# Kernel optimization log

Hardware: AMD Instinct MI355X
Metric: run time of the kernel (lower is better)

## Reference

```python
import jax, jax.numpy as jnp
import numpy as np
from jax import lax
import math

B, C, L, H, K, NCONV = 64, 128, 400, 8, 7, 4  # batch, d_model, length, n_head, kernel, n_conv
DK = C // H
EPS = 1e-5


def setup_inputs() -> dict:
    key = jax.random.key(0)
    ks = jax.random.split(key, 16)
    inp = {
        'x': jax.random.normal(ks[0], (B, C, L), dtype=jnp.float32),
        'mask': jnp.ones((B, L), dtype=jnp.float32),
        'dw_w': jax.random.normal(ks[1], (NCONV, C, 1, K), dtype=jnp.float32) * 0.1,
        'dw_b': jnp.zeros((NCONV, C), dtype=jnp.float32),
        'pw_w': jax.random.normal(ks[2], (NCONV, C, C, 1), dtype=jnp.float32) * 0.05,
        'pw_b': jnp.zeros((NCONV, C), dtype=jnp.float32),
        'wq': jax.random.normal(ks[3], (C, C), dtype=jnp.float32) * 0.05,
        'bq': jnp.zeros((C,), dtype=jnp.float32),
        'wk': jax.random.normal(ks[4], (C, C), dtype=jnp.float32) * 0.05,
        'bk': jnp.zeros((C,), dtype=jnp.float32),
        'wv': jax.random.normal(ks[5], (C, C), dtype=jnp.float32) * 0.05,
        'bv': jnp.zeros((C,), dtype=jnp.float32),
        'wo': jax.random.normal(ks[6], (C, C), dtype=jnp.float32) * 0.05,
        'bo': jnp.zeros((C,), dtype=jnp.float32),
        'fc_w': jax.random.normal(ks[7], (C, C), dtype=jnp.float32) * 0.05,
        'fc_b': jnp.zeros((C,), dtype=jnp.float32),
        'ln_g': jnp.ones((C, L), dtype=jnpp.float32) if False else jnp.ones((C, L), dtype=jnp.float32),
        'ln_b': jnp.zeros((C, L), dtype=jnp.float32),
    }
    return inp


def _pos_encoding():
    i = jnp.arange(C, dtype=jnp.float32)
    even = (jnp.arange(C) % 2) == 0
    freqs = jnp.where(even, 10000.0 ** (-i / C), -(10000.0 ** ((1.0 - i) / C)))
    phases = jnp.where(even, 0.0, math.pi / 2.0)
    pos = jnp.arange(L, dtype=jnp.float32)
    return jnp.sin(pos[None, :] * freqs[:, None] + phases[:, None])  # (C, L)


def _layer_norm(o, g, b):
    # torch LayerNorm([d_model, length]): normalize each sample over (C, L) jointly
    mu = jnp.mean(o, axis=(1, 2), keepdims=True)
    var = jnp.mean((o - mu) ** 2, axis=(1, 2), keepdims=True)
    return (o - mu) * lax.rsqrt(var + EPS) * g[None] + b[None]


def _dwsep_conv(o, dw, db, pw, pb):
    # depthwise: groups=C, kernel (C,1,K), 'same' padding
    y = lax.conv_general_dilated(o, dw, window_strides=(1,), padding=[(K // 2, K // 2)],
                                 dimension_numbers=('NCH', 'OIH', 'NCH'), feature_group_count=C)
    y = y + db[None, :, None]
    # pointwise 1x1 conv
    y = jnp.einsum('oc,bcl->bol', pw[:, :, 0], y) + pb[None, :, None]
    return y


def _attention(o, mask, wq, bq, wk, bk, wv, bv, wo, bo):
    xt = jnp.transpose(o, (0, 2, 1))  # (B, L, C)
    q = (xt @ wq.T + bq).reshape(B, L, H, DK)
    k = (xt @ wk.T + bk).reshape(B, L, H, DK)
    v = (xt @ wv.T + bv).reshape(B, L, H, DK)
    atten = jnp.einsum('blhd,bmhd->bhlm', q, k) / math.sqrt(C)  # note: sqrt(d_model), faithful
    m = mask[:, None, None, :]  # (B,1,1,L)
    atten = atten * m + (1.0 - m) * -1e30
    atten = jax.nn.softmax(atten, axis=-1)
    out = jnp.einsum('bhlm,bmhd->blhd', atten, v).reshape(B, L, C)
    out = out @ wo.T + bo
    return jnp.transpose(out, (0, 2, 1))  # (B, C, L)


def reference(x, mask, dw_w, dw_b, pw_w, pw_b, wq, bq, wk, bk, wv, bv, wo, bo, fc_w, fc_b, ln_g, ln_b):
    out = x + _pos_encoding()[None]
    res = out
    out = _layer_norm(out, ln_g, ln_b)
    for i in range(NCONV):
        out = _dwsep_conv(out, dw_w[i], dw_b[i], pw_w[i], pw_b[i])
        out = jax.nn.relu(out)
        out = res + out
        res = out
        out = _layer_norm(out, ln_g, ln_b)
    out = _attention(out, mask, wq, bq, wk, bk, wv, bv, wo, bo)
    out = res + out
    res = out
    out = _layer_norm(out, ln_g, ln_b)
    out = jnp.einsum('bcl,ec->bel', out, fc_w) + fc_b[None, :, None]
    out = jax.nn.relu(out)
    out = res + out
    return out
```

## Files before the change

### kernel.cpp

```cpp
#include <hip/hip_runtime.h>
#include <math.h>

constexpr int BN = 64;
constexpr int CC = 128;
constexpr int LL = 400;
constexpr int DK = 16;
constexpr int KK = 7;
constexpr int CL = CC * LL;
constexpr int NBCL = BN * CL;
constexpr float EPSV = 1e-5f;
constexpr float INV_N = 1.0f / (float)CL;
constexpr float BIGL = 1.4427e30f;

typedef __attribute__((ext_vector_type(8))) short bf16x8;
typedef __attribute__((ext_vector_type(4))) float f32x4;

__device__ __forceinline__ short f2bf(float f) {
  unsigned u = __builtin_bit_cast(unsigned, f);
  u = (u + 0x7fffu + ((u >> 16) & 1u)) >> 16;
  return (short)u;
}
__device__ __forceinline__ unsigned pkbf(float hi, float lo) {
  return __builtin_amdgcn_perm(__builtin_bit_cast(unsigned, hi),
                               __builtin_bit_cast(unsigned, lo), 0x07060302u);
}

__global__ __launch_bounds__(256) void prep_kernel(
    const float* __restrict__ pw_w, const float* __restrict__ wq,
    const float* __restrict__ wk, const float* __restrict__ wv,
    const float* __restrict__ wo, const float* __restrict__ fcw,
    const float* __restrict__ pw_b, const float* __restrict__ dw_b,
    const float* __restrict__ mask,
    unsigned short* __restrict__ wf, float* __restrict__ pose,
    float* __restrict__ stats, float* __restrict__ beff,
    float* __restrict__ maddb)
{
  int blk = blockIdx.x;
  if (blk < 576) {
    int idx = blk * 256 + threadIdx.x;
    int mat = idx >> 14;
    int e = idx & 16383;
    const float* src;
    if (mat < 4)       src = pw_w + mat * 16384;
    else if (mat == 4) src = wq;
    else if (mat == 5) src = wk;
    else if (mat == 6) src = wv;
    else if (mat == 7) src = wo;
    else               src = fcw;
    int o = e >> 7, c = e & 127;
    int t = (o >> 4) * 4 + (c >> 5);
    int quad = (c >> 3) & 3, col = o & 15, j = c & 7;
    wf[mat * 16384 + t * 512 + (quad * 16 + col) * 8 + j] = (unsigned short)f2bf(src[e]);
  } else if (blk < 776) {
    int idx = (blk - 576) * 256 + threadIdx.x;
    int c = idx / LL, l = idx - c * LL;
    float fc = (float)c;
    float freq, ph;
    if ((c & 1) == 0) { freq = powf(10000.f, -fc / (float)CC);        ph = 0.f; }
    else              { freq = -powf(10000.f, (1.f - fc) / (float)CC); ph = 1.5707963267948966f; }
    pose[idx] = sinf((float)l * freq + ph);
  } else if (blk == 776) {
    for (int i = threadIdx.x; i < 1024; i += 256) stats[i] = 0.f;
  } else if (blk == 777) {
    for (int t = threadIdx.x; t < 512; t += 256) {
      int i = t >> 7, o = t & 127;
      float a = pw_b[t];
      const float* wrow = pw_w + (size_t)i * 16384 + o * 128;
      const float* db = dw_b + i * 128;
      for (int c2 = 0; c2 < 128; c2++) a += wrow[c2] * db[c2];
      beff[t] = a;
    }
  } else {
    int idx = (blk - 778) * 256 + threadIdx.x;
    int b = idx / 416, m = idx - b * 416;
    maddb[idx] = (m < LL) ? (mask[b * LL + m] - 1.f) * BIGL : -BIGL;
  }
}

__global__ __launch_bounds__(256) void addpos_stats_kernel(
    const float* __restrict__ x, const float* __restrict__ pose,
    float* __restrict__ res, float* __restrict__ stats)
{
  int idx4 = blockIdx.x * 256 + threadIdx.x;
  int b = idx4 / (CL / 4);
  int cl4 = (idx4 - b * (CL / 4)) * 4;
  const float4 xv = *reinterpret_cast<const float4*>(&x[(size_t)idx4 * 4]);
  const float4 pv = *reinterpret_cast<const float4*>(&pose[cl4]);
  float4 v = make_float4(xv.x + pv.x, xv.y + pv.y, xv.z + pv.z, xv.w + pv.w);
  *reinterpret_cast<float4*>(&res[(size_t)idx4 * 4]) = v;
  float s1 = v.x + v.y + v.z + v.w;
  float s2 = v.x * v.x + v.y * v.y + v.z * v.z + v.w * v.w;
  #pragma unroll
  for (int off = 32; off > 0; off >>= 1) {
    s1 += __shfl_down(s1, off);
    s2 += __shfl_down(s2, off);
  }
  __shared__ float r1[4], r2[4];
  int wv = threadIdx.x >> 6, lane = threadIdx.x & 63;
  if (lane == 0) { r1[wv] = s1; r2[wv] = s2; }
  __syncthreads();
  if (threadIdx.x == 0) {
    atomicAdd(&stats[b * 2 + 0], r1[0] + r1[1] + r1[2] + r1[3]);
    atomicAdd(&stats[b * 2 + 1], r2[0] + r2[1] + r2[2] + r2[3]);
  }
}

template<int XMODE, int OMODE, bool RELU, bool ADDRES, bool STATS>
__device__ __forceinline__ void gemm_body(
    const unsigned short* __restrict__ Wf, const void* __restrict__ Xv,
    const float* __restrict__ bias, const float* __restrict__ resid,
    const float* __restrict__ lng, const float* __restrict__ lnb,
    const float* __restrict__ dww,
    const float* __restrict__ statsIn, float* __restrict__ statsOut,
    void* __restrict__ Yv)
{
  __shared__ short XsF[16 * 512];
  __shared__ float red[16];
  int tid = threadIdx.x;
  int bb = blockIdx.y;
  int j0 = blockIdx.x * 64;
  int w = tid >> 6, lane = tid & 63;
  bf16x8 af[4];
  #pragma unroll
  for (int kt = 0; kt < 4; kt++)
    af[kt] = *reinterpret_cast<const bf16x8*>(&Wf[(w * 4 + kt) * 512 + lane * 8]);
  float mu = 0.f, rstd = 0.f;
  if (XMODE != 1) {
    float s1 = statsIn[bb * 2 + 0], s2 = statsIn[bb * 2 + 1];
    mu = s1 * INV_N;
    rstd = rsqrtf(s2 * INV_N - mu * mu + EPSV);
  }
  for (int idx = tid; idx < 2048; idx += 512) {
    int c = idx >> 4;
    int l4 = (idx & 15) * 4;
    int col0 = j0 + l4;
    short hv[4] = {0, 0, 0, 0};
    if (XMODE == 2) {
      const float* rp = (const float*)Xv + (size_t)bb * CL + c * LL;
      const float* gp = lng + c * LL;
      const float* bp = lnb + c * LL;
      float xn[12];
      #pragma unroll
      for (int g3 = 0; g3 < 3; g3++) {
        int p0 = col0 - 4 + g3 * 4;
        int pc = p0 < 0 ? 0 : (p0 > LL - 4 ? LL - 4 : p0);
        const float4 rv = *reinterpret_cast<const float4*>(&rp[pc]);
        const float4 gv = *reinterpret_cast<const float4*>(&gp[pc]);
        const float4 bv4 = *reinterpret_cast<const float4*>(&bp[pc]);
        float rr[4] = {rv.x, rv.y, rv.z, rv.w};
        float gg[4] = {gv.x, gv.y, gv.z, gv.w};
        float bbv[4] = {bv4.x, bv4.y, bv4.z, bv4.w};
        #pragma unroll
        for (int e = 0; e < 4; e++) {
          int p = p0 + e;
          float v = (rr[e] - mu) * rstd * gg[e] + bbv[e];
          xn[g3 * 4 + e] = (p >= 0 && p < LL) ? v : 0.f;
        }
      }
      float w7[KK];
      #pragma unroll
      for (int j = 0; j < KK; j++) w7[j] = dww[c * KK + j];
      #pragma unroll
      for (int e = 0; e < 4; e++) {
        float a = 0.f;
        #pragma unroll
        for (int j = 0; j < KK; j++) a += w7[j] * xn[e + j + 1];
        hv[e] = f2bf(a);
      }
    } else if (col0 < LL) {
      if (XMODE == 1) {
        const unsigned short* Xb = (const unsigned short*)Xv + (size_t)bb * CL;
        ushort4 u = *reinterpret_cast<const ushort4*>(&Xb[c * LL + col0]);
        hv[0] = (short)u.x; hv[1] = (short)u.y; hv[2] = (short)u.z; hv[3] = (short)u.w;
      } else {
        const float* Xb = (const float*)Xv + (size_t)bb * CL;
        float4 v = *reinterpret_cast<const float4*>(&Xb[c * LL + col0]);
        const float4 g = *reinterpret_cast<const float4*>(&lng[c * LL + col0]);
        const float4 bt = *reinterpret_cast<const float4*>(&lnb[c * LL + col0]);
        v.x = (v.x - mu) * rstd * g.x + bt.x;
        v.y = (v.y - mu) * rstd * g.y + bt.y;
        v.z = (v.z - mu) * rstd * g.z + bt.z;
        v.w = (v.w - mu) * rstd * g.w + bt.w;
        hv[0] = f2bf(v.x); hv[1] = f2bf(v.y); hv[2] = f2bf(v.z); hv[3] = f2bf(v.w);
      }
    }
    int t = (l4 >> 4) * 4 + (c >> 5);
    int quad = (c >> 3) & 3;
    int j = c & 7;
    int base = t * 512 + quad * 128 + j;
    int colb = l4 & 15;
    #pragma unroll
    for (int e = 0; e < 4; e++) XsF[base + (colb + e) * 8] = hv[e];
  }
  __syncthreads();
  int col = lane & 15, quad = lane >> 4;
  f32x4 acc[4];
  #pragma unroll
  for (int lf = 0; lf < 4; lf++) acc[lf] = (f32x4){0.f, 0.f, 0.f, 0.f};
  #pragma unroll
  for (int kt = 0; kt < 4; kt++) {
    #pragma unroll
    for (int lf = 0; lf < 4; lf++) {
      bf16x8 bx = *reinterpret_cast<const bf16x8*>(&XsF[(lf * 4 + kt) * 512 + lane * 8]);
      acc[lf] = __builtin_amdgcn_mfma_f32_16x16x32_bf16(af[kt], bx, acc[lf], 0, 0, 0);
    }
  }
  int obase = w * 16;
  float bv[4];
  #pragma unroll
  for (int r = 0; r < 4; r++) bv[r] = bias[obase + quad * 4 + r];
  float lsum = 0.f, lsq = 0.f;
  #pragma unroll
  for (int lf = 0; lf < 4; lf++) {
    if (j0 + lf * 16 < LL) {
      int l = j0 + lf * 16 + col;
      if (OMODE == 2) {
        short4 hv4 = {f2bf(acc[lf][0] + bv[0]), f2bf(acc[lf][1] + bv[1]),
                      f2bf(acc[lf][2] + bv[2]), f2bf(acc[lf][3] + bv[3])};
        *reinterpret_cast<short4*>(
            &((unsigned short*)Yv)[(((size_t)bb * 8 + w) * LL + l) * 16 + quad * 4]) = hv4;
      } else {
        #pragma unroll
        for (int r = 0; r < 4; r++) {
          float v = acc[lf][r] + bv[r];
          if (RELU) v = fmaxf(v, 0.f);
          size_t oidx = (size_t)bb * CL + (size_t)(obase + quad * 4 + r) * LL + l;
          if (ADDRES) v += resid[oidx];
          if (OMODE == 1) ((unsigned short*)Yv)[oidx] = (unsigned short)f2bf(v);
          else            ((float*)Yv)[oidx] = v;
          if (STATS) { lsum += v; lsq += v * v; }
        }
      }
    }
  }
  if (STATS) {
    #pragma unroll
    for (int off = 32; off > 0; off >>= 1) {
      lsum += __shfl_down(lsum, off);
      lsq  += __shfl_down(lsq, off);
    }
    if (lane == 0) { red[w * 2] = lsum; red[w * 2 + 1] = lsq; }
    __syncthreads();
    if (tid == 0) {
      float a = 0.f, b2 = 0.f;
      #pragma unroll
      for (int w2 = 0; w2 < 8; w2++) { a += red[w2 * 2]; b2 += red[w2 * 2 + 1]; }
      atomicAdd(&statsOut[bb * 2 + 0], a);
      atomicAdd(&statsOut[bb * 2 + 1], b2);
    }
  }
}

template<int XMODE, int OMODE, bool RELU, bool ADDRES, bool STATS>
__global__ __launch_bounds__(512) void gemmM(
    const unsigned short* __restrict__ Wf, const void* __restrict__ X,
    const float* __restrict__ bias, const float* __restrict__ resid,
    const float* __restrict__ lng, const float* __restrict__ lnb,
    const float* __restrict__ dww,
    const float* __restrict__ statsIn, float* __restrict__ statsOut,
    void* __restrict__ Y)
{
  gemm_body<XMODE, OMODE, RELU, ADDRES, STATS>(
      Wf, X, bias, resid, lng, lnb, dww, statsIn, statsOut, Y);
}

__global__ __launch_bounds__(512) void qkv_kernel(
    const unsigned short* __restrict__ wf,
    const float* __restrict__ bq, const float* __restrict__ bk, const float* __restrict__ bv,
    const float* __restrict__ X,
    const float* __restrict__ lng, const float* __restrict__ lnb,
    const float* __restrict__ statsIn,
    unsigned short* __restrict__ qt, unsigned short* __restrict__ kt,
    unsigned short* __restrict__ vb)
{
  if (blockIdx.z == 0)
    gemm_body<0, 2, false, false, false>(wf + 4 * 16384, X, bq, nullptr, lng, lnb,
                                         nullptr, statsIn, nullptr, qt);
  else if (blockIdx.z == 1)
    gemm_body<0, 2, false, false, false>(wf + 5 * 16384, X, bk, nullptr, lng, lnb,
                                         nullptr, statsIn, nullptr, kt);
  else
    gemm_body<0, 1, false, false, false>(wf + 6 * 16384, X, bv, nullptr, lng, lnb,
                                         nullptr, statsIn, nullptr, vb);
}

__global__ __launch_bounds__(64, 4) void attn_kernel(
    const unsigned short* __restrict__ qt, const unsigned short* __restrict__ kt,
    const unsigned short* __restrict__ vb, const float* __restrict__ maddb,
    unsigned short* __restrict__ ao)
{
  __shared__ short Pl[2][64 * 40];
  int bh = blockIdx.x;
  int b = bh >> 3, h = bh & 7;
  int lane = threadIdx.x;
  int col = lane & 15;
  int quad = lane >> 4;
  int l0 = blockIdx.y * 64;
  size_t trow = ((size_t)b * 8 + h) * LL;
  size_t base = ((size_t)b * CC + h * DK) * LL;
  const unsigned short* qp = qt + trow * 16;
  const unsigned short* kp = kt + trow * 16;
  const unsigned short* vp = vb + base;
  const float* mb = maddb + (size_t)b * 416;

  bf16x8 qf[4];
  #pragma unroll
  for (int f = 0; f < 4; f++) {
    bf16x8 v = {};
    if (quad < 2) {
      int l = l0 + f * 16 + col; int lc = l < LL ? l : LL - 1;
      v = *reinterpret_cast<const bf16x8*>(&qp[lc * 16 + quad * 8]);
    }
    qf[f] = v;
  }
  f32x4 of[4];
  float psum[4];
  #pragma unroll
  for (int f = 0; f < 4; f++) {
    of[f] = (f32x4){0.f, 0.f, 0.f, 0.f};
    psum[f] = 0.f;
  }
  const float scale2 = 0.08838834764831845f * 1.4426950408889634f;

  int buf = 0;
  for (int m0 = 0; m0 < LL; m0 += 32, buf ^= 1) {
    bf16x8 kf0 = {}, kf1 = {};
    if (quad < 2) {
      int mc0 = m0 + col < LL ? m0 + col : LL - 1;
      int mc1 = m0 + 16 + col < LL ? m0 + 16 + col : LL - 1;
      kf0 = *reinterpret_cast<const bf16x8*>(&kp[mc0 * 16 + quad * 8]);
      kf1 = *reinterpret_cast<const bf16x8*>(&kp[mc1 * 16 + quad * 8]);
    }
    bf16x8 vf;
    {
      int ms = m0 + quad * 8; if (ms > LL - 8) ms = LL - 8;
      vf = *reinterpret_cast<const bf16x8*>(&vp[col * LL + ms]);
    }
    const float4 a4 = *reinterpret_cast<const float4*>(&mb[m0 + quad * 4]);
    const float4 b4 = *reinterpret_cast<const float4*>(&mb[m0 + 16 + quad * 4]);
    float madd[8] = {a4.x, a4.y, a4.z, a4.w, b4.x, b4.y, b4.z, b4.w};
    #pragma unroll
    for (int f = 0; f < 4; f++) {
      f32x4 z = {0.f, 0.f, 0.f, 0.f};
      f32x4 s0 = __builtin_amdgcn_mfma_f32_16x16x32_bf16(kf0, qf[f], z, 0, 0, 0);
      f32x4 s1 = __builtin_amdgcn_mfma_f32_16x16x32_bf16(kf1, qf[f], z, 0, 0, 0);
      float p[8];
      #pragma unroll
      for (int r = 0; r < 4; r++) {
        p[r]     = exp2f(s0[r] * scale2 + madd[r]);
        p[4 + r] = exp2f(s1[r] * scale2 + madd[4 + r]);
      }
      float ps = 0.f;
      #pragma unroll
      for (int i = 0; i < 8; i++) ps += p[i];
      psum[f] += ps;
      short* row = &Pl[buf][(f * 16 + col) * 40];
      short4 h0 = __builtin_bit_cast(short4, make_uint2(pkbf(p[1], p[0]), pkbf(p[3], p[2])));
      short4 h1 = __builtin_bit_cast(short4, make_uint2(pkbf(p[5], p[4]), pkbf(p[7], p[6])));
      *reinterpret_cast<short4*>(&row[quad * 4])      = h0;
      *reinterpret_cast<short4*>(&row[16 + quad * 4]) = h1;
    }
    #pragma unroll
    for (int f = 0; f < 4; f++) {
      bf16x8 pf = *reinterpret_cast<const bf16x8*>(&Pl[buf][(f * 16 + col) * 40 + quad * 8]);
      of[f] = __builtin_amdgcn_mfma_f32_16x16x32_bf16(vf, pf, of[f], 0, 0, 0);
    }
  }
  #pragma unroll
  for (int f = 0; f < 4; f++) {
    float s = psum[f];
    s += __shfl_xor(s, 16);
    s += __shfl_xor(s, 32);
    float inv = 1.f / s;
    int lf = l0 + f * 16;
    if (lf < LL) {
      #pragma unroll
      for (int r = 0; r < 4; r++)
        ao[base + (size_t)(quad * 4 + r) * LL + lf + col] =
            (unsigned short)f2bf(of[f][r] * inv);
    }
  }
}

extern "C" void kernel_launch(void* const* d_in, const int* in_sizes, int n_in,
                              void* d_out, int out_size, void* d_ws, size_t ws_size,
                              hipStream_t stream) {
  const float* x    = (const float*)d_in[0];
  const float* mask = (const float*)d_in[1];
  const float* dw_w = (const float*)d_in[2];
  const float* dw_b = (const float*)d_in[3];
  const float* pw_w = (const float*)d_in[4];
  const float* pw_b = (const float*)d_in[5];
  const float* wq   = (const float*)d_in[6];
  const float* bq   = (const float*)d_in[7];
  const float* wk   = (const float*)d_in[8];
  const float* bk   = (const float*)d_in[9];
  const float* wvp  = (const float*)d_in[10];
  const float* bv   = (const float*)d_in[11];
  const float* wo   = (const float*)d_in[12];
  const float* bo   = (const float*)d_in[13];
  const float* fcw  = (const float*)d_in[14];
  const float* fcb  = (const float*)d_in[15];
  const float* lng  = (const float*)d_in[16];
  const float* lnb  = (const float*)d_in[17];
  float* out = (float*)d_out;
  float* ws  = (float*)d_ws;

  float* stats = ws;
  float* pose  = ws + 1024;
  float* beff  = pose + 51200;
  float* maddb = beff + 512;
  unsigned short* wf = (unsigned short*)(maddb + 64 * 416);
  float* res = (float*)(wf + 9 * 16384);
  unsigned short* qt = (unsigned short*)(res + NBCL);
  unsigned short* kt = qt + NBCL;
  unsigned short* vb = kt + NBCL;
  unsigned short* tb = vb + NBCL;

  prep_kernel<<<882, 256, 0, stream>>>(pw_w, wq, wk, wvp, wo, fcw, pw_b, dw_b,
                                       mask, wf, pose, stats, beff, maddb);
  addpos_stats_kernel<<<3200, 256, 0, stream>>>(x, pose, res, stats);

  for (int i = 0; i < 4; i++) {
    gemmM<2, 0, true, true, true><<<dim3(7, BN), 512, 0, stream>>>(
        wf + i * 16384, res, beff + i * CC, res, lng, lnb,
        dw_w + i * CC * KK, stats + i * 128, stats + (i + 1) * 128, res);
  }
  qkv_kernel<<<dim3(7, BN, 3), 512, 0, stream>>>(
      wf, bq, bk, bv, res, lng, lnb, stats + 4 * 128, qt, kt, vb);
  attn_kernel<<<dim3(512, 7), 64, 0, stream>>>(qt, kt, vb, maddb, tb);
  gemmM<1, 0, false, true, true><<<dim3(7, BN), 512, 0, stream>>>(
      wf + 7 * 16384, tb, bo, res, nullptr, nullptr, nullptr,
      nullptr, stats + 5 * 128, res);
  gemmM<0, 0, true, true, false><<<dim3(7, BN), 512, 0, stream>>>(
      wf + 8 * 16384, res, fcb, res, lng, lnb, nullptr,
      stats + 5 * 128, nullptr, out);
}
```

Measured before the change: 262.5 us.

## Fuse QKV projections to share staged X tile, widen conv staging, pack attention waves

The QKV kernel now stages the layer-normed input tile into shared memory once and runs all three projections (Q, K, V) from it, instead of three separate blocks each re-reading and normalising the same input. The depthwise-conv staging path processes 8 outputs per thread with a 16-element window, which cuts redundant halo loads. The attention kernel packs four 64-row tiles per 256-thread block, each wave with its own shared buffer. The trade-offs are a third as many QKV blocks with serial per-block work, and one wasted wave per head in attention, since 7 tiles are spread over 8 wave slots.

```diff
diff --git a/kernel.cpp b/kernel.cpp
--- a/kernel.cpp
+++ b/kernel.cpp
@@ -105,44 +105,24 @@
   }
 }
 
-template<int XMODE, int OMODE, bool RELU, bool ADDRES, bool STATS>
-__device__ __forceinline__ void gemm_body(
-    const unsigned short* __restrict__ Wf, const void* __restrict__ Xv,
-    const float* __restrict__ bias, const float* __restrict__ resid,
+template<int XMODE>
+__device__ __forceinline__ void stage_x(
+    short* __restrict__ XsF, const void* __restrict__ Xv, int bb, int j0,
     const float* __restrict__ lng, const float* __restrict__ lnb,
-    const float* __restrict__ dww,
-    const float* __restrict__ statsIn, float* __restrict__ statsOut,
-    void* __restrict__ Yv)
-{
-  __shared__ short XsF[16 * 512];
-  __shared__ float red[16];
-  int tid = threadIdx.x;
-  int bb = blockIdx.y;
-  int j0 = blockIdx.x * 64;
-  int w = tid >> 6, lane = tid & 63;
-  bf16x8 af[4];
-  #pragma unroll
-  for (int kt = 0; kt < 4; kt++)
-    af[kt] = *reinterpret_cast<const bf16x8*>(&Wf[(w * 4 + kt) * 512 + lane * 8]);
-  float mu = 0.f, rstd = 0.f;
-  if (XMODE != 1) {
-    float s1 = statsIn[bb * 2 + 0], s2 = statsIn[bb * 2 + 1];
-    mu = s1 * INV_N;
-    rstd = rsqrtf(s2 * INV_N - mu * mu + EPSV);
-  }
-  for (int idx = tid; idx < 2048; idx += 512) {
-    int c = idx >> 4;
-    int l4 = (idx & 15) * 4;
-    int col0 = j0 + l4;
-    short hv[4] = {0, 0, 0, 0};
-    if (XMODE == 2) {
+    const float* __restrict__ dww, float mu, float rstd, int tid)
+{
+  if (XMODE == 2) {
+    for (int idx = tid; idx < 1024; idx += 512) {
+      int c = idx >> 3;
+      int l8 = (idx & 7) * 8;
+      int col0 = j0 + l8;
       const float* rp = (const float*)Xv + (size_t)bb * CL + c * LL;
       const float* gp = lng + c * LL;
       const float* bp = lnb + c * LL;
-      float xn[12];
-      #pragma unroll
-      for (int g3 = 0; g3 < 3; g3++) {
-        int p0 = col0 - 4 + g3 * 4;
+      float xn[16];
+      #pragma unroll
+      for (int g4 = 0; g4 < 4; g4++) {
+        int p0 = col0 - 4 + g4 * 4;
         int pc = p0 < 0 ? 0 : (p0 > LL - 4 ? LL - 4 : p0);
         const float4 rv = *reinterpret_cast<const float4*>(&rp[pc]);
         const float4 gv = *reinterpret_cast<const float4*>(&gp[pc]);
@@ -154,44 +134,85 @@
         for (int e = 0; e < 4; e++) {
           int p = p0 + e;
           float v = (rr[e] - mu) * rstd * gg[e] + bbv[e];
-          xn[g3 * 4 + e] = (p >= 0 && p < LL) ? v : 0.f;
+          xn[g4 * 4 + e] = (p >= 0 && p < LL) ? v : 0.f;
         }
       }
       float w7[KK];
       #pragma unroll
       for (int j = 0; j < KK; j++) w7[j] = dww[c * KK + j];
-      #pragma unroll
-      for (int e = 0; e < 4; e++) {
+      int t = (l8 >> 4) * 4 + (c >> 5);
+      int quad = (c >> 3) & 3;
+      int j = c & 7;
+      int base = t * 512 + quad * 128 + j;
+      int colb = l8 & 15;
+      #pragma unroll
+      for (int e = 0; e < 8; e++) {
         float a = 0.f;
         #pragma unroll
-        for (int j = 0; j < KK; j++) a += w7[j] * xn[e + j + 1];
-        hv[e] = f2bf(a);
-      }
-    } else if (col0 < LL) {
-      if (XMODE == 1) {
-        const unsigned short* Xb = (const unsigned short*)Xv + (size_t)bb * CL;
-        ushort4 u = *reinterpret_cast<const ushort4*>(&Xb[c * LL + col0]);
-        hv[0] = (short)u.x; hv[1] = (short)u.y; hv[2] = (short)u.z; hv[3] = (short)u.w;
-      } else {
-        const float* Xb = (const float*)Xv + (size_t)bb * CL;
-        float4 v = *reinterpret_cast<const float4*>(&Xb[c * LL + col0]);
-        const float4 g = *reinterpret_cast<const float4*>(&lng[c * LL + col0]);
-        const float4 bt = *reinterpret_cast<const float4*>(&lnb[c * LL + col0]);
-        v.x = (v.x - mu) * rstd * g.x + bt.x;
-        v.y = (v.y - mu) * rstd * g.y + bt.y;
-        v.z = (v.z - mu) * rstd * g.z + bt.z;
-        v.w = (v.w - mu) * rstd * g.w + bt.w;
-        hv[0] = f2bf(v.x); hv[1] = f2bf(v.y); hv[2] = f2bf(v.z); hv[3] = f2bf(v.w);
-      }
-    }
-    int t = (l4 >> 4) * 4 + (c >> 5);
-    int quad = (c >> 3) & 3;
-    int j = c & 7;
-    int base = t * 512 + quad * 128 + j;
-    int colb = l4 & 15;
-    #pragma unroll
-    for (int e = 0; e < 4; e++) XsF[base + (colb + e) * 8] = hv[e];
-  }
+        for (int jj = 0; jj < KK; jj++) a += w7[jj] * xn[e + jj + 1];
+        XsF[base + (colb + e) * 8] = f2bf(a);
+      }
+    }
+  } else {
+    for (int idx = tid; idx < 2048; idx += 512) {
+      int c = idx >> 4;
+      int l4 = (idx & 15) * 4;
+      int col0 = j0 + l4;
+      short hv[4] = {0, 0, 0, 0};
+      if (col0 < LL) {
+        if (XMODE == 1) {
+          const unsigned short* Xb = (const unsigned short*)Xv + (size_t)bb * CL;
+          ushort4 u = *reinterpret_cast<const ushort4*>(&Xb[c * LL + col0]);
+          hv[0] = (short)u.x; hv[1] = (short)u.y; hv[2] = (short)u.z; hv[3] = (short)u.w;
+        } else {
+          const float* Xb = (const float*)Xv + (size_t)bb * CL;
+          float4 v = *reinterpret_cast<const float4*>(&Xb[c * LL + col0]);
+          const float4 g = *reinterpret_cast<const float4*>(&lng[c * LL + col0]);
+          const float4 bt = *reinterpret_cast<const float4*>(&lnb[c * LL + col0]);
+          v.x = (v.x - mu) * rstd * g.x + bt.x;
+          v.y = (v.y - mu) * rstd * g.y + bt.y;
+          v.z = (v.z - mu) * rstd * g.z + bt.z;
+          v.w = (v.w - mu) * rstd * g.w + bt.w;
+          hv[0] = f2bf(v.x); hv[1] = f2bf(v.y); hv[2] = f2bf(v.z); hv[3] = f2bf(v.w);
+        }
+      }
+      int t = (l4 >> 4) * 4 + (c >> 5);
+      int quad = (c >> 3) & 3;
+      int j = c & 7;
+      int base = t * 512 + quad * 128 + j;
+      int colb = l4 & 15;
+      #pragma unroll
+      for (int e = 0; e < 4; e++) XsF[base + (colb + e) * 8] = hv[e];
+    }
+  }
+}
+
+template<int XMODE, int OMODE, bool RELU, bool ADDRES, bool STATS>
+__device__ __forceinline__ void gemm_body(
+    const unsigned short* __restrict__ Wf, const void* __restrict__ Xv,
+    const float* __restrict__ bias, const float* __restrict__ resid,
+    const float* __restrict__ lng, const float* __restrict__ lnb,
+    const float* __restrict__ dww,
+    const float* __restrict__ statsIn, float* __restrict__ statsOut,
+    void* __restrict__ Yv)
+{
+  __shared__ short XsF[16 * 512];
+  __shared__ float red[16];
+  int tid = threadIdx.x;
+  int bb = blockIdx.y;
+  int j0 = blockIdx.x * 64;
+  int w = tid >> 6, lane = tid & 63;
+  bf16x8 af[4];
+  #pragma unroll
+  for (int kt = 0; kt < 4; kt++)
+    af[kt] = *reinterpret_cast<const bf16x8*>(&Wf[(w * 4 + kt) * 512 + lane * 8]);
+  float mu = 0.f, rstd = 0.f;
+  if (XMODE != 1) {
+    float s1 = statsIn[bb * 2 + 0], s2 = statsIn[bb * 2 + 1];
+    mu = s1 * INV_N;
+    rstd = rsqrtf(s2 * INV_N - mu * mu + EPSV);
+  }
+  stage_x<XMODE>(XsF, Xv, bb, j0, lng, lnb, dww, mu, rstd, tid);
   __syncthreads();
   int col = lane & 15, quad = lane >> 4;
   f32x4 acc[4];
@@ -273,29 +294,76 @@
     unsigned short* __restrict__ qt, unsigned short* __restrict__ kt,
     unsigned short* __restrict__ vb)
 {
-  if (blockIdx.z == 0)
-    gemm_body<0, 2, false, false, false>(wf + 4 * 16384, X, bq, nullptr, lng, lnb,
-                                         nullptr, statsIn, nullptr, qt);
-  else if (blockIdx.z == 1)
-    gemm_body<0, 2, false, false, false>(wf + 5 * 16384, X, bk, nullptr, lng, lnb,
-                                         nullptr, statsIn, nullptr, kt);
-  else
-    gemm_body<0, 1, false, false, false>(wf + 6 * 16384, X, bv, nullptr, lng, lnb,
-                                         nullptr, statsIn, nullptr, vb);
-}
-
-__global__ __launch_bounds__(64, 4) void attn_kernel(
+  __shared__ short XsF[16 * 512];
+  int tid = threadIdx.x;
+  int bb = blockIdx.y;
+  int j0 = blockIdx.x * 64;
+  int w = tid >> 6, lane = tid & 63;
+  float s1 = statsIn[bb * 2 + 0], s2 = statsIn[bb * 2 + 1];
+  float mu = s1 * INV_N;
+  float rstd = rsqrtf(s2 * INV_N - mu * mu + EPSV);
+  stage_x<0>(XsF, X, bb, j0, lng, lnb, nullptr, mu, rstd, tid);
+  __syncthreads();
+  int col = lane & 15, quad = lane >> 4;
+  #pragma unroll
+  for (int m = 0; m < 3; m++) {
+    const unsigned short* Wf = wf + (4 + m) * 16384;
+    const float* bias = (m == 0) ? bq : (m == 1) ? bk : bv;
+    bf16x8 af[4];
+    #pragma unroll
+    for (int kt2 = 0; kt2 < 4; kt2++)
+      af[kt2] = *reinterpret_cast<const bf16x8*>(&Wf[(w * 4 + kt2) * 512 + lane * 8]);
+    f32x4 acc[4];
+    #pragma unroll
+    for (int lf = 0; lf < 4; lf++) acc[lf] = (f32x4){0.f, 0.f, 0.f, 0.f};
+    #pragma unroll
+    for (int kt2 = 0; kt2 < 4; kt2++) {
+      #pragma unroll
+      for (int lf = 0; lf < 4; lf++) {
+        bf16x8 bx = *reinterpret_cast<const bf16x8*>(&XsF[(lf * 4 + kt2) * 512 + lane * 8]);
+        acc[lf] = __builtin_amdgcn_mfma_f32_16x16x32_bf16(af[kt2], bx, acc[lf], 0, 0, 0);
+      }
+    }
+    int obase = w * 16;
+    float bvv[4];
+    #pragma unroll
+    for (int r = 0; r < 4; r++) bvv[r] = bias[obase + quad * 4 + r];
+    #pragma unroll
+    for (int lf = 0; lf < 4; lf++) {
+      if (j0 + lf * 16 < LL) {
+        int l = j0 + lf * 16 + col;
+        if (m < 2) {
+          unsigned short* Y = (m == 0) ? qt : kt;
+          short4 hv4 = {f2bf(acc[lf][0] + bvv[0]), f2bf(acc[lf][1] + bvv[1]),
+                        f2bf(acc[lf][2] + bvv[2]), f2bf(acc[lf][3] + bvv[3])};
+          *reinterpret_cast<short4*>(
+              &Y[(((size_t)bb * 8 + w) * LL + l) * 16 + quad * 4]) = hv4;
+        } else {
+          #pragma unroll
+          for (int r = 0; r < 4; r++) {
+            size_t oidx = (size_t)bb * CL + (size_t)(obase + quad * 4 + r) * LL + l;
+            vb[oidx] = (unsigned short)f2bf(acc[lf][r] + bvv[r]);
+          }
+        }
+      }
+    }
+  }
+}
+
+__global__ __launch_bounds__(256) void attn_kernel(
     const unsigned short* __restrict__ qt, const unsigned short* __restrict__ kt,
     const unsigned short* __restrict__ vb, const float* __restrict__ maddb,
     unsigned short* __restrict__ ao)
 {
-  __shared__ short Pl[2][64 * 40];
+  __shared__ short Pl[4][2][64 * 40];
   int bh = blockIdx.x;
   int b = bh >> 3, h = bh & 7;
-  int lane = threadIdx.x;
+  int wave = threadIdx.x >> 6, lane = threadIdx.x & 63;
+  int tile = blockIdx.y * 4 + wave;
+  if (tile >= 7) return;
   int col = lane & 15;
   int quad = lane >> 4;
-  int l0 = blockIdx.y * 64;
+  int l0 = tile * 64;
   size_t trow = ((size_t)b * 8 + h) * LL;
   size_t base = ((size_t)b * CC + h * DK) * LL;
   const unsigned short* qp = qt + trow * 16;
@@ -354,7 +422,7 @@
       #pragma unroll
       for (int i = 0; i < 8; i++) ps += p[i];
       psum[f] += ps;
-      short* row = &Pl[buf][(f * 16 + col) * 40];
+      short* row = &Pl[wave][buf][(f * 16 + col) * 40];
       short4 h0 = __builtin_bit_cast(short4, make_uint2(pkbf(p[1], p[0]), pkbf(p[3], p[2])));
       short4 h1 = __builtin_bit_cast(short4, make_uint2(pkbf(p[5], p[4]), pkbf(p[7], p[6])));
       *reinterpret_cast<short4*>(&row[quad * 4])      = h0;
@@ -362,7 +430,7 @@
     }
     #pragma unroll
     for (int f = 0; f < 4; f++) {
-      bf16x8 pf = *reinterpret_cast<const bf16x8*>(&Pl[buf][(f * 16 + col) * 40 + quad * 8]);
+      bf16x8 pf = *reinterpret_cast<const bf16x8*>(&Pl[wave][buf][(f * 16 + col) * 40 + quad * 8]);
       of[f] = __builtin_amdgcn_mfma_f32_16x16x32_bf16(vf, pf, of[f], 0, 0, 0);
     }
   }
@@ -426,9 +494,9 @@
         wf + i * 16384, res, beff + i * CC, res, lng, lnb,
         dw_w + i * CC * KK, stats + i * 128, stats + (i + 1) * 128, res);
   }
-  qkv_kernel<<<dim3(7, BN, 3), 512, 0, stream>>>(
+  qkv_kernel<<<dim3(7, BN), 512, 0, stream>>>(
       wf, bq, bk, bv, res, lng, lnb, stats + 4 * 128, qt, kt, vb);
-  attn_kernel<<<dim3(512, 7), 64, 0, stream>>>(qt, kt, vb, maddb, tb);
+  attn_kernel<<<dim3(512, 2), 256, 0, stream>>>(qt, kt, vb, maddb, tb);
   gemmM<1, 0, false, true, true><<<dim3(7, BN), 512, 0, stream>>>(
       wf + 7 * 16384, tb, bo, res, nullptr, nullptr, nullptr,
       nullptr, stats + 5 * 128, res);
```

Measured after the change: 265.7 us. No clear change (+1.2%).

## Store residual stream in bf16 with ping-pong buffers and pack attention waves

Applied to the files above, without the earlier changes.

Stores the residual activations as bf16 instead of fp32 throughout the conv, attention and output stages, using two ping-pong buffers so each GEMM no longer reads and writes the same array in place. LayerNorm statistics are accumulated from the rounded bf16 values. The X staging loop now handles 8 columns per thread. Attention launches 4 waves per block, each with its own LDS tile. The aim is to roughly halve residual memory traffic, at the cost of accumulating bf16 rounding error across the five residual additions.

```diff
diff --git a/kernel.cpp b/kernel.cpp
--- a/kernel.cpp
+++ b/kernel.cpp
@@ -19,6 +19,9 @@
   unsigned u = __builtin_bit_cast(unsigned, f);
   u = (u + 0x7fffu + ((u >> 16) & 1u)) >> 16;
   return (short)u;
+}
+__device__ __forceinline__ float bf2f(unsigned short u) {
+  return __builtin_bit_cast(float, (unsigned)u << 16);
 }
 __device__ __forceinline__ unsigned pkbf(float hi, float lo) {
   return __builtin_amdgcn_perm(__builtin_bit_cast(unsigned, hi),
@@ -79,17 +82,22 @@
 
 __global__ __launch_bounds__(256) void addpos_stats_kernel(
     const float* __restrict__ x, const float* __restrict__ pose,
-    float* __restrict__ res, float* __restrict__ stats)
+    unsigned short* __restrict__ res, float* __restrict__ stats)
 {
   int idx4 = blockIdx.x * 256 + threadIdx.x;
   int b = idx4 / (CL / 4);
   int cl4 = (idx4 - b * (CL / 4)) * 4;
   const float4 xv = *reinterpret_cast<const float4*>(&x[(size_t)idx4 * 4]);
   const float4 pv = *reinterpret_cast<const float4*>(&pose[cl4]);
-  float4 v = make_float4(xv.x + pv.x, xv.y + pv.y, xv.z + pv.z, xv.w + pv.w);
-  *reinterpret_cast<float4*>(&res[(size_t)idx4 * 4]) = v;
-  float s1 = v.x + v.y + v.z + v.w;
-  float s2 = v.x * v.x + v.y * v.y + v.z * v.z + v.w * v.w;
+  ushort4 h;
+  h.x = (unsigned short)f2bf(xv.x + pv.x);
+  h.y = (unsigned short)f2bf(xv.y + pv.y);
+  h.z = (unsigned short)f2bf(xv.z + pv.z);
+  h.w = (unsigned short)f2bf(xv.w + pv.w);
+  *reinterpret_cast<ushort4*>(&res[(size_t)idx4 * 4]) = h;
+  float v0 = bf2f(h.x), v1 = bf2f(h.y), v2 = bf2f(h.z), v3 = bf2f(h.w);
+  float s1 = v0 + v1 + v2 + v3;
+  float s2 = v0 * v0 + v1 * v1 + v2 * v2 + v3 * v3;
   #pragma unroll
   for (int off = 32; off > 0; off >>= 1) {
     s1 += __shfl_down(s1, off);
@@ -105,10 +113,89 @@
   }
 }
 
+template<int XMODE>
+__device__ __forceinline__ void stage_x(
+    short* __restrict__ XsF, const unsigned short* __restrict__ Xb,
+    int j0, const float* __restrict__ lng, const float* __restrict__ lnb,
+    const float* __restrict__ dww, float mu, float rstd, int tid)
+{
+  for (int idx = tid; idx < 1024; idx += 512) {
+    int c = idx >> 3;
+    int l8 = (idx & 7) * 8;
+    int col0 = j0 + l8;
+    short hv[8];
+    if (XMODE == 2) {
+      const unsigned short* rp = Xb + c * LL;
+      const float* gp = lng + c * LL;
+      const float* bp = lnb + c * LL;
+      float xn[16];
+      #pragma unroll
+      for (int g4 = 0; g4 < 4; g4++) {
+        int p0 = col0 - 4 + g4 * 4;
+        int pc = p0 < 0 ? 0 : (p0 > LL - 4 ? LL - 4 : p0);
+        const ushort4 rv = *reinterpret_cast<const ushort4*>(&rp[pc]);
+        const float4 gv = *reinterpret_cast<const float4*>(&gp[pc]);
+        const float4 bv4 = *reinterpret_cast<const float4*>(&bp[pc]);
+        float rr[4] = {bf2f(rv.x), bf2f(rv.y), bf2f(rv.z), bf2f(rv.w)};
+        float gg[4] = {gv.x, gv.y, gv.z, gv.w};
+        float bbv[4] = {bv4.x, bv4.y, bv4.z, bv4.w};
+        #pragma unroll
+        for (int e = 0; e < 4; e++) {
+          int p = p0 + e;
+          float v = (rr[e] - mu) * rstd * gg[e] + bbv[e];
+          xn[g4 * 4 + e] = (p >= 0 && p < LL) ? v : 0.f;
+        }
+      }
+      float w7[KK];
+      #pragma unroll
+      for (int j = 0; j < KK; j++) w7[j] = dww[c * KK + j];
+      #pragma unroll
+      for (int e = 0; e < 8; e++) {
+        float a = 0.f;
+        #pragma unroll
+        for (int jj = 0; jj < KK; jj++) a += w7[jj] * xn[e + jj + 1];
+        hv[e] = f2bf(a);
+      }
+    } else {
+      bool valid = col0 < LL;
+      int col0c = valid ? col0 : 0;
+      const unsigned short* xp = Xb + c * LL + col0c;
+      const ushort4 u0 = *reinterpret_cast<const ushort4*>(&xp[0]);
+      const ushort4 u1 = *reinterpret_cast<const ushort4*>(&xp[4]);
+      unsigned short uu[8] = {u0.x, u0.y, u0.z, u0.w, u1.x, u1.y, u1.z, u1.w};
+      if (XMODE == 1) {
+        #pragma unroll
+        for (int e = 0; e < 8; e++) hv[e] = valid ? (short)uu[e] : (short)0;
+      } else {
+        const float* gp = lng + c * LL + col0c;
+        const float* bp = lnb + c * LL + col0c;
+        const float4 g0 = *reinterpret_cast<const float4*>(&gp[0]);
+        const float4 g1 = *reinterpret_cast<const float4*>(&gp[4]);
+        const float4 b0 = *reinterpret_cast<const float4*>(&bp[0]);
+        const float4 b1 = *reinterpret_cast<const float4*>(&bp[4]);
+        float gg[8] = {g0.x, g0.y, g0.z, g0.w, g1.x, g1.y, g1.z, g1.w};
+        float bbv[8] = {b0.x, b0.y, b0.z, b0.w, b1.x, b1.y, b1.z, b1.w};
+        #pragma unroll
+        for (int e = 0; e < 8; e++) {
+          float v = (bf2f(uu[e]) - mu) * rstd * gg[e] + bbv[e];
+          hv[e] = valid ? f2bf(v) : (short)0;
+        }
+      }
+    }
+    int t = (l8 >> 4) * 4 + (c >> 5);
+    int quad = (c >> 3) & 3;
+    int j = c & 7;
+    int base = t * 512 + quad * 128 + j;
+    int colb = l8 & 15;
+    #pragma unroll
+    for (int e = 0; e < 8; e++) XsF[base + (colb + e) * 8] = hv[e];
+  }
+}
+
 template<int XMODE, int OMODE, bool RELU, bool ADDRES, bool STATS>
 __device__ __forceinline__ void gemm_body(
-    const unsigned short* __restrict__ Wf, const void* __restrict__ Xv,
-    const float* __restrict__ bias, const float* __restrict__ resid,
+    const unsigned short* __restrict__ Wf, const unsigned short* __restrict__ Xv,
+    const float* __restrict__ bias, const unsigned short* __restrict__ resid,
     const float* __restrict__ lng, const float* __restrict__ lnb,
     const float* __restrict__ dww,
     const float* __restrict__ statsIn, float* __restrict__ statsOut,
@@ -130,68 +217,7 @@
     mu = s1 * INV_N;
     rstd = rsqrtf(s2 * INV_N - mu * mu + EPSV);
   }
-  for (int idx = tid; idx < 2048; idx += 512) {
-    int c = idx >> 4;
-    int l4 = (idx & 15) * 4;
-    int col0 = j0 + l4;
-    short hv[4] = {0, 0, 0, 0};
-    if (XMODE == 2) {
-      const float* rp = (const float*)Xv + (size_t)bb * CL + c * LL;
-      const float* gp = lng + c * LL;
-      const float* bp = lnb + c * LL;
-      float xn[12];
-      #pragma unroll
-      for (int g3 = 0; g3 < 3; g3++) {
-        int p0 = col0 - 4 + g3 * 4;
-        int pc = p0 < 0 ? 0 : (p0 > LL - 4 ? LL - 4 : p0);
-        const float4 rv = *reinterpret_cast<const float4*>(&rp[pc]);
-        const float4 gv = *reinterpret_cast<const float4*>(&gp[pc]);
-        const float4 bv4 = *reinterpret_cast<const float4*>(&bp[pc]);
-        float rr[4] = {rv.x, rv.y, rv.z, rv.w};
-        float gg[4] = {gv.x, gv.y, gv.z, gv.w};
-        float bbv[4] = {bv4.x, bv4.y, bv4.z, bv4.w};
-        #pragma unroll
-        for (int e = 0; e < 4; e++) {
-          int p = p0 + e;
-          float v = (rr[e] - mu) * rstd * gg[e] + bbv[e];
-          xn[g3 * 4 + e] = (p >= 0 && p < LL) ? v : 0.f;
-        }
-      }
-      float w7[KK];
-      #pragma unroll
-      for (int j = 0; j < KK; j++) w7[j] = dww[c * KK + j];
-      #pragma unroll
-      for (int e = 0; e < 4; e++) {
-        float a = 0.f;
-        #pragma unroll
-        for (int j = 0; j < KK; j++) a += w7[j] * xn[e + j + 1];
-        hv[e] = f2bf(a);
-      }
-    } else if (col0 < LL) {
-      if (XMODE == 1) {
-        const unsigned short* Xb = (const unsigned short*)Xv + (size_t)bb * CL;
-        ushort4 u = *reinterpret_cast<const ushort4*>(&Xb[c * LL + col0]);
-        hv[0] = (short)u.x; hv[1] = (short)u.y; hv[2] = (short)u.z; hv[3] = (short)u.w;
-      } else {
-        const float* Xb = (const float*)Xv + (size_t)bb * CL;
-        float4 v = *reinterpret_cast<const float4*>(&Xb[c * LL + col0]);
-        const float4 g = *reinterpret_cast<const float4*>(&lng[c * LL + col0]);
-        const float4 bt = *reinterpret_cast<const float4*>(&lnb[c * LL + col0]);
-        v.x = (v.x - mu) * rstd * g.x + bt.x;
-        v.y = (v.y - mu) * rstd * g.y + bt.y;
-        v.z = (v.z - mu) * rstd * g.z + bt.z;
-        v.w = (v.w - mu) * rstd * g.w + bt.w;
-        hv[0] = f2bf(v.x); hv[1] = f2bf(v.y); hv[2] = f2bf(v.z); hv[3] = f2bf(v.w);
-      }
-    }
-    int t = (l4 >> 4) * 4 + (c >> 5);
-    int quad = (c >> 3) & 3;
-    int j = c & 7;
-    int base = t * 512 + quad * 128 + j;
-    int colb = l4 & 15;
-    #pragma unroll
-    for (int e = 0; e < 4; e++) XsF[base + (colb + e) * 8] = hv[e];
-  }
+  stage_x<XMODE>(XsF, Xv + (size_t)bb * CL, j0, lng, lnb, dww, mu, rstd, tid);
   __syncthreads();
   int col = lane & 15, quad = lane >> 4;
   f32x4 acc[4];
@@ -225,10 +251,15 @@
           float v = acc[lf][r] + bv[r];
           if (RELU) v = fmaxf(v, 0.f);
           size_t oidx = (size_t)bb * CL + (size_t)(obase + quad * 4 + r) * LL + l;
-          if (ADDRES) v += resid[oidx];
-          if (OMODE == 1) ((unsigned short*)Yv)[oidx] = (unsigned short)f2bf(v);
-          else            ((float*)Yv)[oidx] = v;
-          if (STATS) { lsum += v; lsq += v * v; }
+          if (ADDRES) v += bf2f(resid[oidx]);
+          if (OMODE == 1) {
+            unsigned short hb = (unsigned short)f2bf(v);
+            ((unsigned short*)Yv)[oidx] = hb;
+            if (STATS) { float vf = bf2f(hb); lsum += vf; lsq += vf * vf; }
+          } else {
+            ((float*)Yv)[oidx] = v;
+            if (STATS) { lsum += v; lsq += v * v; }
+          }
         }
       }
     }
@@ -253,8 +284,8 @@
 
 template<int XMODE, int OMODE, bool RELU, bool ADDRES, bool STATS>
 __global__ __launch_bounds__(512) void gemmM(
-    const unsigned short* __restrict__ Wf, const void* __restrict__ X,
-    const float* __restrict__ bias, const float* __restrict__ resid,
+    const unsigned short* __restrict__ Wf, const unsigned short* __restrict__ X,
+    const float* __restrict__ bias, const unsigned short* __restrict__ resid,
     const float* __restrict__ lng, const float* __restrict__ lnb,
     const float* __restrict__ dww,
     const float* __restrict__ statsIn, float* __restrict__ statsOut,
@@ -267,7 +298,7 @@
 __global__ __launch_bounds__(512) void qkv_kernel(
     const unsigned short* __restrict__ wf,
     const float* __restrict__ bq, const float* __restrict__ bk, const float* __restrict__ bv,
-    const float* __restrict__ X,
+    const unsigned short* __restrict__ X,
     const float* __restrict__ lng, const float* __restrict__ lnb,
     const float* __restrict__ statsIn,
     unsigned short* __restrict__ qt, unsigned short* __restrict__ kt,
@@ -284,18 +315,20 @@
                                          nullptr, statsIn, nullptr, vb);
 }
 
-__global__ __launch_bounds__(64, 4) void attn_kernel(
+__global__ __launch_bounds__(256) void attn_kernel(
     const unsigned short* __restrict__ qt, const unsigned short* __restrict__ kt,
     const unsigned short* __restrict__ vb, const float* __restrict__ maddb,
     unsigned short* __restrict__ ao)
 {
-  __shared__ short Pl[2][64 * 40];
+  __shared__ short Pl[4][2][64 * 40];
   int bh = blockIdx.x;
   int b = bh >> 3, h = bh & 7;
-  int lane = threadIdx.x;
+  int wave = threadIdx.x >> 6, lane = threadIdx.x & 63;
+  int tile = blockIdx.y * 4 + wave;
+  if (tile >= 7) return;
   int col = lane & 15;
   int quad = lane >> 4;
-  int l0 = blockIdx.y * 64;
+  int l0 = tile * 64;
   size_t trow = ((size_t)b * 8 + h) * LL;
   size_t base = ((size_t)b * CC + h * DK) * LL;
   const unsigned short* qp = qt + trow * 16;
@@ -354,7 +387,7 @@
       #pragma unroll
       for (int i = 0; i < 8; i++) ps += p[i];
       psum[f] += ps;
-      short* row = &Pl[buf][(f * 16 + col) * 40];
+      short* row = &Pl[wave][buf][(f * 16 + col) * 40];
       short4 h0 = __builtin_bit_cast(short4, make_uint2(pkbf(p[1], p[0]), pkbf(p[3], p[2])));
       short4 h1 = __builtin_bit_cast(short4, make_uint2(pkbf(p[5], p[4]), pkbf(p[7], p[6])));
       *reinterpret_cast<short4*>(&row[quad * 4])      = h0;
@@ -362,7 +395,7 @@
     }
     #pragma unroll
     for (int f = 0; f < 4; f++) {
-      bf16x8 pf = *reinterpret_cast<const bf16x8*>(&Pl[buf][(f * 16 + col) * 40 + quad * 8]);
+      bf16x8 pf = *reinterpret_cast<const bf16x8*>(&Pl[wave][buf][(f * 16 + col) * 40 + quad * 8]);
       of[f] = __builtin_amdgcn_mfma_f32_16x16x32_bf16(vf, pf, of[f], 0, 0, 0);
     }
   }
@@ -411,28 +444,32 @@
   float* beff  = pose + 51200;
   float* maddb = beff + 512;
   unsigned short* wf = (unsigned short*)(maddb + 64 * 416);
-  float* res = (float*)(wf + 9 * 16384);
-  unsigned short* qt = (unsigned short*)(res + NBCL);
+  unsigned short* r0 = wf + 9 * 16384;
+  unsigned short* r1 = r0 + NBCL;
+  unsigned short* qt = r1 + NBCL;
   unsigned short* kt = qt + NBCL;
-  unsigned short* vb = kt + NBCL;
-  unsigned short* tb = vb + NBCL;
+  unsigned short* vbf = kt + NBCL;
+  unsigned short* tb = vbf + NBCL;
 
   prep_kernel<<<882, 256, 0, stream>>>(pw_w, wq, wk, wvp, wo, fcw, pw_b, dw_b,
                                        mask, wf, pose, stats, beff, maddb);
-  addpos_stats_kernel<<<3200, 256, 0, stream>>>(x, pose, res, stats);
-
+  addpos_stats_kernel<<<3200, 256, 0, stream>>>(x, pose, r0, stats);
+
+  unsigned short* rin = r0;
+  unsigned short* rout = r1;
   for (int i = 0; i < 4; i++) {
-    gemmM<2, 0, true, true, true><<<dim3(7, BN), 512, 0, stream>>>(
-        wf + i * 16384, res, beff + i * CC, res, lng, lnb,
-        dw_w + i * CC * KK, stats + i * 128, stats + (i + 1) * 128, res);
+    gemmM<2, 1, true, true, true><<<dim3(7, BN), 512, 0, stream>>>(
+        wf + i * 16384, rin, beff + i * CC, rin, lng, lnb,
+        dw_w + i * CC * KK, stats + i * 128, stats + (i + 1) * 128, rout);
+    unsigned short* t = rin; rin = rout; rout = t;
   }
   qkv_kernel<<<dim3(7, BN, 3), 512, 0, stream>>>(
-      wf, bq, bk, bv, res, lng, lnb, stats + 4 * 128, qt, kt, vb);
-  attn_kernel<<<dim3(512, 7), 64, 0, stream>>>(qt, kt, vb, maddb, tb);
-  gemmM<1, 0, false, true, true><<<dim3(7, BN), 512, 0, stream>>>(
-      wf + 7 * 16384, tb, bo, res, nullptr, nullptr, nullptr,
-      nullptr, stats + 5 * 128, res);
+      wf, bq, bk, bv, rin, lng, lnb, stats + 4 * 128, qt, kt, vbf);
+  attn_kernel<<<dim3(512, 2), 256, 0, stream>>>(qt, kt, vbf, maddb, tb);
+  gemmM<1, 1, false, true, true><<<dim3(7, BN), 512, 0, stream>>>(
+      wf + 7 * 16384, tb, bo, rin, nullptr, nullptr, nullptr,
+      nullptr, stats + 5 * 128, rout);
   gemmM<0, 0, true, true, false><<<dim3(7, BN), 512, 0, stream>>>(
-      wf + 8 * 16384, res, fcb, res, lng, lnb, nullptr,
+      wf + 8 * 16384, rout, fcb, rout, lng, lnb, nullptr,
       stats + 5 * 128, nullptr, out);
 }
```

Result: no change. 262.2 us (-0.1%).
